# Performance work log

Measured on AMD Instinct MI355X. Metric: run time of the kernel, lower is better.

The kernel has to match this reference:

```python
import jax, jax.numpy as jnp
import numpy as np

B, S, HIST, D, NH, L = 8, 1024, 128, 1024, 16, 6
SD, TD, AD = 10, 3, 5
DH = D // NH
FF = 4 * D
EPS = 1e-5
SCALE = 1.0 / np.sqrt(DH)


def posenc(T):
    # sinusoidal PE, matches PositionalEncoding (positions start at 0)
    pos = jnp.arange(T, dtype=jnp.float32)[:, None]
    div = jnp.exp(jnp.arange(0, D, 2, dtype=jnp.float32) * (-np.log(10000.0) / D))
    pe = jnp.zeros((T, D), jnp.float32)
    pe = pe.at[:, 0::2].set(jnp.sin(pos * div))
    pe = pe.at[:, 1::2].set(jnp.cos(pos * div))
    return pe


def layernorm(x, g, b):
    m = jnp.mean(x, -1, keepdims=True)
    v = jnp.var(x, -1, keepdims=True)
    return (x - m) * jax.lax.rsqrt(v + EPS) * g + b


def mlp2(u, w1, b1, w2, b2):
    # Linear -> SiLU -> Linear (ConditionEmbedding branch)
    return jax.nn.silu(u @ w1 + b1) @ w2 + b2


def mha(q_in, kv_in, wq, bq, wk, bk, wv, bv, wo, bo, mask):
    Bq, Tq, _ = q_in.shape
    Tk = kv_in.shape[1]
    q = (q_in @ wq + bq).reshape(Bq, Tq, NH, DH)
    k = (kv_in @ wk + bk).reshape(Bq, Tk, NH, DH)
    v = (kv_in @ wv + bv).reshape(Bq, Tk, NH, DH)
    s = jnp.einsum('bthd,bshd->bhts', q, k) * SCALE + mask
    a = jax.nn.softmax(s, axis=-1)
    o = jnp.einsum('bhts,bshd->bthd', a, v).reshape(Bq, Tq, D)
    return o @ wo + bo


def setup_inputs():
    key = jax.random.key(0)
    ki = iter(jax.random.split(key, 64))
    w = lambda *sh: jax.random.normal(next(ki), sh, jnp.float32) * 0.02
    z = lambda *sh: jnp.zeros(sh, jnp.float32)
    inp = {
        'x': jax.random.normal(next(ki), (B, S, SD), jnp.float32),
        't': jax.random.randint(next(ki), (B,), 0, 30, dtype=jnp.int32),
        'target': jax.random.normal(next(ki), (B, TD), jnp.float32),
        'action': jax.random.normal(next(ki), (B, AD), jnp.float32),
        'history': jax.random.normal(next(ki), (B, HIST, SD), jnp.float32),
        'in_w': w(SD, D), 'in_b': z(D),
        't_w1': w(1, D), 't_b1': z(D), 't_w2': w(D, D), 't_b2': z(D),
        'tg_w1': w(TD, D), 'tg_b1': z(D), 'tg_w2': w(D, D), 'tg_b2': z(D),
        'ac_w1': w(AD, D), 'ac_b1': z(D), 'ac_w2': w(D, D), 'ac_b2': z(D),
        'sa_wq': w(L, D, D), 'sa_bq': z(L, D), 'sa_wk': w(L, D, D), 'sa_bk': z(L, D),
        'sa_wv': w(L, D, D), 'sa_bv': z(L, D), 'sa_wo': w(L, D, D), 'sa_bo': z(L, D),
        'ca_wq': w(L, D, D), 'ca_bq': z(L, D), 'ca_wk': w(L, D, D), 'ca_bk': z(L, D),
        'ca_wv': w(L, D, D), 'ca_bv': z(L, D), 'ca_wo': w(L, D, D), 'ca_bo': z(L, D),
        'ln1_g': jnp.ones((L, D), jnp.float32), 'ln1_b': z(L, D),
        'ln2_g': jnp.ones((L, D), jnp.float32), 'ln2_b': z(L, D),
        'ln3_g': jnp.ones((L, D), jnp.float32), 'ln3_b': z(L, D),
        'ff_w1': w(L, D, FF), 'ff_b1': z(L, FF), 'ff_w2': w(L, FF, D), 'ff_b2': z(L, D),
        'out_w': w(D, SD), 'out_b': z(SD),
    }
    return inp


def reference(x, t, target, action, history, in_w, in_b,
              t_w1, t_b1, t_w2, t_b2, tg_w1, tg_b1, tg_w2, tg_b2,
              ac_w1, ac_b1, ac_w2, ac_b2,
              sa_wq, sa_bq, sa_wk, sa_bk, sa_wv, sa_bv, sa_wo, sa_bo,
              ca_wq, ca_bq, ca_wk, ca_bk, ca_wv, ca_bv, ca_wo, ca_bo,
              ln1_g, ln1_b, ln2_g, ln2_b, ln3_g, ln3_b,
              ff_w1, ff_b1, ff_w2, ff_b2, out_w, out_b):
    # embed current traj and history (PE applied to each separately, as in torch code)
    x_emb = x @ in_w + in_b + posenc(S)[None]
    h_emb = history @ in_w + in_b + posenc(HIST)[None]
    # condition embedding: t + target + action branches
    cond = (mlp2(t[:, None].astype(jnp.float32), t_w1, t_b1, t_w2, t_b2)
            + mlp2(target, tg_w1, tg_b1, tg_w2, tg_b2)
            + mlp2(action, ac_w1, ac_b1, ac_w2, ac_b2))
    z = jnp.concatenate([h_emb, x_emb], axis=1) + cond[:, None, :]  # [B, T, D]
    T = HIST + S
    mask = jnp.where(jnp.tril(jnp.ones((T, T), bool)), 0.0, -jnp.inf)[None, None]
    mem = z  # TransformerDecoder memory is the (fixed) input sequence
    for i in range(L):
        # post-LN TransformerDecoderLayer: self-attn, cross-attn, relu FFN
        z = layernorm(z + mha(z, z, sa_wq[i], sa_bq[i], sa_wk[i], sa_bk[i],
                              sa_wv[i], sa_bv[i], sa_wo[i], sa_bo[i], mask), ln1_g[i], ln1_b[i])
        z = layernorm(z + mha(z, mem, ca_wq[i], ca_bq[i], ca_wk[i], ca_bk[i],
                              ca_wv[i], ca_bv[i], ca_wo[i], ca_bo[i], mask), ln2_g[i], ln2_b[i])
        ff = jax.nn.relu(z @ ff_w1[i] + ff_b1[i]) @ ff_w2[i] + ff_b2[i]
        z = layernorm(z + ff, ln3_g[i], ln3_b[i])
    return z[:, -S:, :] @ out_w + out_b
```

## Files before the change

### kernel.cpp

```cpp
#include <hip/hip_runtime.h>
#include <hip/hip_bf16.h>
#include <stdint.h>

#define B_    8
#define S_    1024
#define HIST_ 128
#define T_    1152
#define D_    1024
#define NH_   16
#define DH_   64
#define FF_   4096
#define L_    6
#define NROWS_ (B_*T_)

typedef __attribute__((ext_vector_type(8))) __bf16 bf16x8;
typedef __attribute__((ext_vector_type(4))) __bf16 bf16x4;
typedef __attribute__((ext_vector_type(4))) float  f32x4;

static __device__ __forceinline__ f32x4 mfma16(bf16x8 a, bf16x8 b, f32x4 c) {
  return __builtin_amdgcn_mfma_f32_16x16x32_bf16(a, b, c, 0, 0, 0);
}
static __device__ __forceinline__ void gload16(const __bf16* g, __bf16* l) {
  __builtin_amdgcn_global_load_lds((const __attribute__((address_space(1))) void*)g,
                                   (__attribute__((address_space(3))) void*)l, 16, 0, 0);
}
static __device__ __forceinline__ void gload16b(const char* g, char* l) {
  __builtin_amdgcn_global_load_lds((const __attribute__((address_space(1))) void*)g,
                                   (__attribute__((address_space(3))) void*)l, 16, 0, 0);
}
static __device__ __forceinline__ int xcd_swz(int orig, int nwg) {
  const int q = nwg >> 3, r = nwg & 7;
  const int x = orig & 7, i = orig >> 3;
  return (x < r ? x*(q+1) : r*(q+1) + (x-r)*q) + i;
}

template<int BF16OUT, int RELU>
__global__ __launch_bounds__(512, 2) void gemm192_k(const __bf16* __restrict__ A,
                                                    const __bf16* __restrict__ Bt,
                                                    const float* __restrict__ bias,
                                                    void* __restrict__ Cout,
                                                    int M, int N, int K, int ldc) {
  __shared__ __align__(16) char Lds[2][57344];
  const int tid = threadIdx.x;
  const int wid = tid >> 6, ln = tid & 63;
  const int wm = wid >> 2, wn = wid & 3;
  const int l15 = ln & 15, g = ln >> 4;
  const int nbx = N >> 8;
  const int wg = xcd_swz(blockIdx.x, gridDim.x);
  const int m0 = (wg / nbx) * 192, n0 = (wg % nbx) << 8;
  const size_t rstep = (size_t)K * 2;

  const char* srcp[7];
  int dsto[7];
#pragma unroll
  for (int p = 0; p < 7; ++p) {
    const int off = p*8192 + tid*16;
    int mat, ks, row;
    if (off < 12288)      { mat = 0; ks = 0; row = off >> 6; }
    else if (off < 24576) { mat = 0; ks = 1; row = (off - 12288) >> 6; }
    else if (off < 40960) { mat = 1; ks = 0; row = (off - 24576) >> 6; }
    else                  { mat = 1; ks = 1; row = (off - 40960) >> 6; }
    const int ch = (off >> 4) & 3;
    const int kb = ks*64 + ((ch ^ ((row >> 1) & 3)) << 4);
    srcp[p] = (mat ? (const char*)Bt + (size_t)(n0 + row)*rstep
                   : (const char*)A  + (size_t)(m0 + row)*rstep) + kb;
    dsto[p] = off;
  }
  auto stage = [&](int buf, int t) {
    char* lb = &Lds[buf][0];
    const size_t tb = (size_t)t << 7;
#pragma unroll
    for (int p = 0; p < 7; ++p) gload16b(srcp[p] + tb, lb + dsto[p]);
  };

  const int xr = (g ^ ((l15 >> 1) & 3)) << 4;
  const int arow = l15*64 + xr;
  const int aoffm = (wm*96) * 64;
  const int boff  = 24576 + (wn*64) * 64;

  const f32x4 zero = {0.f,0.f,0.f,0.f};
  f32x4 acc[6][4];
#pragma unroll
  for (int i=0;i<6;i++)
#pragma unroll
    for (int j=0;j<4;j++) acc[i][j] = zero;

  stage(0, 0); stage(1, 1);

  const int NT = K >> 6;
  for (int t = 0; t < NT; ++t) {
    const int buf = t & 1;
    if (t == NT-1) { asm volatile("s_waitcnt vmcnt(0)" ::: "memory"); }
    else           { asm volatile("s_waitcnt vmcnt(7)" ::: "memory"); }
    __builtin_amdgcn_s_barrier();
    const char* bufp = &Lds[buf][0];
    bf16x8 a0[6], a1[6], b0[4], b1[4];
#pragma unroll
    for (int mi=0;mi<6;mi++) a0[mi] = *(const bf16x8*)(bufp + aoffm + mi*1024 + arow);
#pragma unroll
    for (int ni=0;ni<4;ni++) b0[ni] = *(const bf16x8*)(bufp + boff + ni*1024 + arow);
#pragma unroll
    for (int mi=0;mi<6;mi++) a1[mi] = *(const bf16x8*)(bufp + 12288 + aoffm + mi*1024 + arow);
    __builtin_amdgcn_s_setprio(1);
#pragma unroll
    for (int mi=0;mi<6;mi++)
#pragma unroll
      for (int ni=0;ni<4;ni++) acc[mi][ni] = mfma16(a0[mi], b0[ni], acc[mi][ni]);
    __builtin_amdgcn_s_setprio(0);
#pragma unroll
    for (int ni=0;ni<4;ni++) b1[ni] = *(const bf16x8*)(bufp + boff + 16384 + ni*1024 + arow);
    asm volatile("s_waitcnt lgkmcnt(0)" ::: "memory");
    __builtin_amdgcn_sched_barrier(0);
    __builtin_amdgcn_s_barrier();
    if (t + 2 <= NT - 1) stage(buf, t + 2);
    __builtin_amdgcn_s_setprio(1);
#pragma unroll
    for (int mi=0;mi<6;mi++)
#pragma unroll
      for (int ni=0;ni<4;ni++) acc[mi][ni] = mfma16(a1[mi], b1[ni], acc[mi][ni]);
    __builtin_amdgcn_s_setprio(0);
  }

  const int colb = n0 + wn*64 + l15;
#pragma unroll
  for (int mi=0;mi<6;mi++) {
    const int row = m0 + wm*96 + mi*16 + g*4;
#pragma unroll
    for (int ni=0;ni<4;ni++) {
      const int col = colb + ni*16;
      const float bv = bias[col];
#pragma unroll
      for (int j=0;j<4;j++) {
        float v = acc[mi][ni][j] + bv;
        if (RELU) v = fmaxf(v, 0.f);
        if (BF16OUT) ((__bf16*)Cout)[(size_t)(row+j)*ldc + col] = (__bf16)v;
        else         ((float*)Cout)[(size_t)(row+j)*ldc + col] = v;
      }
    }
  }
}

template<int OUTMODE, int RELU>
__global__ __launch_bounds__(512, 2) void gemm256_k(const __bf16* __restrict__ A,
                                                    const __bf16* __restrict__ A2, int asplit,
                                                    const __bf16* __restrict__ Bt,
                                                    const float* __restrict__ b1,
                                                    const float* __restrict__ b2,
                                                    const float* __restrict__ b3, int s1, int s2,
                                                    void* __restrict__ CoutRM,
                                                    __bf16* __restrict__ CoutT,
                                                    int M, int N, int K, int ldc, int tsplit) {
  __shared__ __align__(16) __bf16 Lds[2][2][2][8192];
  const int tid = threadIdx.x;
  const int wid = tid >> 6, ln = tid & 63;
  const int wm = wid >> 2, wn = wid & 3;
  const int l15 = ln & 15, g = ln >> 4;
  const int nbx = N >> 8;
  const int wg = xcd_swz(blockIdx.x, gridDim.x);
  const int m0 = (wg / nbx) << 8, n0 = (wg % nbx) << 8;
  const size_t rstep = (size_t)K * 2;
  const __bf16* Aeff = (n0 < asplit) ? A : A2;

  const int srow = tid >> 2, schunk = tid & 3;
  const int sx = (schunk ^ ((srow >> 1) & 3)) << 4;
  const char* gAr = (const char*)Aeff + (size_t)(m0 + srow)*rstep + sx;
  const char* gBr = (const char*)Bt   + (size_t)(n0 + srow)*rstep + sx;
  const size_t hstep = (size_t)128 * rstep;

  const int xr = (g ^ ((l15 >> 1) & 3)) << 4;
  const int arow = l15 * 64 + xr;
  const int aoffm = (wm*128) * 64;
  const int boff  = (wn*64) * 64;

  const f32x4 zero = {0.f,0.f,0.f,0.f};
  f32x4 acc[8][4];
#pragma unroll
  for (int i=0;i<8;i++)
#pragma unroll
    for (int j=0;j<4;j++) acc[i][j] = zero;

  auto stage4 = [&](int buf, int ks, int tile) {
    const size_t off = (size_t)tile*128 + (size_t)ks*64;
    char* la = (char*)&Lds[buf][ks][0][0];
    char* lb = (char*)&Lds[buf][ks][1][0];
    gload16b(gAr + off,         la + tid*16);
    gload16b(gAr + off + hstep, la + 8192 + tid*16);
    gload16b(gBr + off,         lb + tid*16);
    gload16b(gBr + off + hstep, lb + 8192 + tid*16);
  };

  auto ktile = [&](int buf, bool st, int stile, bool gate0) {
    if (gate0) { asm volatile("s_waitcnt vmcnt(0)" ::: "memory"); }
    else       { asm volatile("s_waitcnt vmcnt(8)" ::: "memory"); }
    __builtin_amdgcn_s_barrier();
    const char* As0 = (const char*)&Lds[buf][0][0][0];
    const char* Bs0 = (const char*)&Lds[buf][0][1][0];
    const char* As1 = (const char*)&Lds[buf][1][0][0];
    const char* Bs1 = (const char*)&Lds[buf][1][1][0];
    bf16x8 a0[4], a1[4], b0[4], a2[4], b1v[4], a3[4];
#pragma unroll
    for (int mi=0;mi<4;mi++) a0[mi] = *(const bf16x8*)(As0 + aoffm + mi*1024 + arow);
#pragma unroll
    for (int ni=0;ni<4;ni++) b0[ni] = *(const bf16x8*)(Bs0 + boff + ni*1024 + arow);
#pragma unroll
    for (int mi=0;mi<4;mi++) a1[mi] = *(const bf16x8*)(As0 + aoffm + 4096 + mi*1024 + arow);
    __builtin_amdgcn_s_setprio(1);
#pragma unroll
    for (int mi=0;mi<4;mi++)
#pragma unroll
      for (int ni=0;ni<4;ni++) acc[mi][ni] = mfma16(a0[mi], b0[ni], acc[mi][ni]);
    __builtin_amdgcn_s_setprio(0);
#pragma unroll
    for (int mi=0;mi<4;mi++) a2[mi]  = *(const bf16x8*)(As1 + aoffm + mi*1024 + arow);
#pragma unroll
    for (int ni=0;ni<4;ni++) b1v[ni] = *(const bf16x8*)(Bs1 + boff + ni*1024 + arow);
    asm volatile("s_waitcnt lgkmcnt(0)" ::: "memory");
    __builtin_amdgcn_s_barrier();
    if (st) stage4(buf, 0, stile);
    __builtin_amdgcn_s_setprio(1);
#pragma unroll
    for (int mi=0;mi<4;mi++)
#pragma unroll
      for (int ni=0;ni<4;ni++) acc[4+mi][ni] = mfma16(a1[mi], b0[ni], acc[4+mi][ni]);
    __builtin_amdgcn_s_setprio(0);
#pragma unroll
    for (int mi=0;mi<4;mi++) a3[mi] = *(const bf16x8*)(As1 + aoffm + 4096 + mi*1024 + arow);
    __builtin_amdgcn_s_setprio(1);
#pragma unroll
    for (int mi=0;mi<4;mi++)
#pragma unroll
      for (int ni=0;ni<4;ni++) acc[mi][ni] = mfma16(a2[mi], b1v[ni], acc[mi][ni]);
    __builtin_amdgcn_s_setprio(0);
    asm volatile("s_waitcnt lgkmcnt(0)" ::: "memory");
    __builtin_amdgcn_s_barrier();
    if (st) stage4(buf, 1, stile);
    __builtin_amdgcn_s_setprio(1);
#pragma unroll
    for (int mi=0;mi<4;mi++)
#pragma unroll
      for (int ni=0;ni<4;ni++) acc[4+mi][ni] = mfma16(a3[mi], b1v[ni], acc[4+mi][ni]);
    __builtin_amdgcn_s_setprio(0);
  };

  stage4(0, 0, 0); stage4(0, 1, 0);
  stage4(1, 0, 1); stage4(1, 1, 1);

  const int NT = K >> 6, NI = NT >> 1;
  for (int i = 0; i < NI; ++i) {
    const bool st = (i + 1 < NI);
    ktile(0, st, 2*i + 2, false);
    ktile(1, st, 2*i + 3, i == NI - 1);
  }

  const int colb = n0 + wn*64 + l15;
#pragma unroll
  for (int mi=0;mi<8;mi++) {
    const int row = m0 + wm*128 + mi*16 + g*4;
#pragma unroll
    for (int ni=0;ni<4;ni++) {
      const int col = colb + ni*16;
      const float bv = (col < s1) ? b1[col] : ((col < s2) ? b2[col-s1] : b3[col-s2]);
      if (OUTMODE == 3 && col >= tsplit) {
        bf16x4 ct;
#pragma unroll
        for (int j=0;j<4;j++) {
          float v = acc[mi][ni][j] + bv;
          if (RELU) v = fmaxf(v, 0.f);
          ct[j] = (__bf16)v;
        }
        *(bf16x4*)(CoutT + (size_t)(col - tsplit)*M + row) = ct;
      } else {
#pragma unroll
        for (int j=0;j<4;j++) {
          float v = acc[mi][ni][j] + bv;
          if (RELU) v = fmaxf(v, 0.f);
          if (OUTMODE == 0) ((float*)CoutRM)[(size_t)(row+j)*ldc + col] = v;
          else              ((__bf16*)CoutRM)[(size_t)(row+j)*ldc + col] = (__bf16)v;
        }
      }
    }
  }
}

__global__ __launch_bounds__(256) void attn_k(const __bf16* __restrict__ QK,
                                              const __bf16* __restrict__ Vt,
                                              __bf16* __restrict__ O) {
  __shared__ __align__(16) __bf16 Ks[2][4096];
  __shared__ __align__(16) __bf16 Vs[2][4096];
  __shared__ __align__(16) __bf16 Pl[4][32*72];
  const int tid = threadIdx.x;
  const int wv = tid >> 6, ln = tid & 63;
  const int l15 = ln & 15, g = ln >> 4;
  const int wg = xcd_swz(blockIdx.x, 1152);
  const int qb = 8 - (wg % 9);
  const int hd = (wg / 9) & 15;
  const int b  = wg / 144;
  const int q0 = qb*128 + wv*32;

  bf16x8 qf[2][2];
#pragma unroll
  for (int f=0; f<2; ++f)
#pragma unroll
    for (int h=0; h<2; ++h)
      qf[f][h] = *(const bf16x8*)(QK + (size_t)(b*T_ + q0 + f*16 + l15)*2048 + hd*64 + h*32 + g*8);

  const int sr = tid >> 3;
  const int si = tid & 7;
  const int cb0 = (si*16) ^ ((sr & 7) << 4);
  const char* kg = (const char*)(QK + (size_t)b*T_*2048 + 1024 + hd*64);
  const char* vg = (const char*)(Vt + (size_t)hd*64*NROWS_ + (size_t)b*T_);

  const f32x4 zero = {0.f,0.f,0.f,0.f};
  f32x4 o[2][4];
#pragma unroll
  for (int f=0; f<2; ++f)
#pragma unroll
    for (int d=0; d<4; ++d) o[f][d] = zero;
  float mrun[2] = {-3.0e38f, -3.0e38f};
  float lrun[2] = {0.f, 0.f};
  const int nt = 2*qb + 2;

  {
    const int c = 0, kt = 0;
#pragma unroll
    for (int hr=0; hr<2; ++hr) {
      const int r = sr + hr*32;
      gload16((const __bf16*)(kg + (size_t)(kt + r)*4096 + cb0), &Ks[c][0] + hr*2048 + wv*512);
      gload16((const __bf16*)(vg + (size_t)r*(NROWS_*2) + (size_t)kt*2 + cb0), &Vs[c][0] + hr*2048 + wv*512);
    }
  }

  for (int t = 0; t < nt; ++t) {
    __syncthreads();
    if (t+1 < nt) {
      const int c = (t+1)&1, kt2 = (t+1)*64;
#pragma unroll
      for (int hr=0; hr<2; ++hr) {
        const int r = sr + hr*32;
        gload16((const __bf16*)(kg + (size_t)(kt2 + r)*4096 + cb0), &Ks[c][0] + hr*2048 + wv*512);
        gload16((const __bf16*)(vg + (size_t)r*(NROWS_*2) + (size_t)kt2*2 + cb0), &Vs[c][0] + hr*2048 + wv*512);
      }
    }
    const int kt = t*64;
    if (kt > q0 + 31) continue;
    const char* ks = (const char*)&Ks[t&1][0];
    const char* vs = (const char*)&Vs[t&1][0];

#pragma unroll
    for (int f=0; f<2; ++f) {
      const int qrow = q0 + f*16 + l15;
      f32x4 st[4];
      __builtin_amdgcn_s_setprio(1);
#pragma unroll
      for (int kf=0; kf<4; ++kf) {
        const int row = kf*16 + l15;
        const int swz = (row & 7) << 4;
        const bf16x8 k0 = *(const bf16x8*)(ks + row*128 + ((g*16) ^ swz));
        const bf16x8 k1 = *(const bf16x8*)(ks + row*128 + ((64 + g*16) ^ swz));
        st[kf] = mfma16(k1, qf[f][1], mfma16(k0, qf[f][0], zero));
      }
      __builtin_amdgcn_s_setprio(0);
      float p[16];
#pragma unroll
      for (int kf=0; kf<4; ++kf)
#pragma unroll
        for (int r=0; r<4; ++r) {
          const int kgl = kt + kf*16 + g*4 + r;
          p[kf*4+r] = (kgl <= qrow) ? st[kf][r]*0.125f : -3.0e38f;
        }
      float mloc = p[0];
#pragma unroll
      for (int i=1;i<16;i++) mloc = fmaxf(mloc, p[i]);
      mloc = fmaxf(mloc, __shfl_xor(mloc, 16));
      mloc = fmaxf(mloc, __shfl_xor(mloc, 32));
      if (__all(mloc - mrun[f] <= 8.f)) {
        float ls = 0.f;
#pragma unroll
        for (int i=0;i<16;i++) { p[i] = __expf(p[i] - mrun[f]); ls += p[i]; }
        ls += __shfl_xor(ls, 16); ls += __shfl_xor(ls, 32);
        lrun[f] += ls;
      } else {
        const float mnew = fmaxf(mrun[f], mloc);
        const float corr = __expf(mrun[f] - mnew);
        float ls = 0.f;
#pragma unroll
        for (int i=0;i<16;i++) { p[i] = __expf(p[i] - mnew); ls += p[i]; }
        ls += __shfl_xor(ls, 16); ls += __shfl_xor(ls, 32);
        lrun[f] = lrun[f]*corr + ls;
        mrun[f] = mnew;
        float cr[4];
#pragma unroll
        for (int r=0;r<4;r++) cr[r] = __shfl(corr, g*4 + r);
#pragma unroll
        for (int db=0; db<4; ++db)
#pragma unroll
          for (int r=0;r<4;r++) o[f][db][r] *= cr[r];
      }
#pragma unroll
      for (int kf=0; kf<4; ++kf) {
        bf16x4 pw;
#pragma unroll
        for (int r=0;r<4;r++) pw[r] = (__bf16)p[kf*4+r];
        *(bf16x4*)(&Pl[wv][(f*16 + l15)*72 + kf*16 + g*4]) = pw;
      }
    }
    __builtin_amdgcn_s_setprio(1);
#pragma unroll
    for (int f=0; f<2; ++f)
#pragma unroll
      for (int ks2=0; ks2<2; ++ks2) {
        const bf16x8 pa = *(const bf16x8*)(&Pl[wv][(f*16 + l15)*72 + ks2*32 + g*8]);
#pragma unroll
        for (int db=0; db<4; ++db) {
          const int d = db*16 + l15;
          const bf16x8 vf = *(const bf16x8*)(vs + d*128 + ((ks2*64 + g*16) ^ ((d & 7) << 4)));
          o[f][db] = mfma16(pa, vf, o[f][db]);
        }
      }
    __builtin_amdgcn_s_setprio(0);
  }

#pragma unroll
  for (int f=0; f<2; ++f) {
    const float inv = 1.f / lrun[f];
    float ir[4];
#pragma unroll
    for (int r=0;r<4;r++) ir[r] = __shfl(inv, g*4 + r);
#pragma unroll
    for (int db=0; db<4; ++db)
#pragma unroll
      for (int r=0;r<4;r++)
        O[(size_t)(b*T_ + q0 + f*16 + g*4 + r)*D_ + hd*64 + db*16 + l15] = (__bf16)(o[f][db][r]*ir[r]);
  }
}

__global__ __launch_bounds__(256) void wprep_k(const float* __restrict__ q, const float* __restrict__ k,
                                               const float* __restrict__ v, const float* __restrict__ o,
                                               const float* __restrict__ cq, const float* __restrict__ ck,
                                               const float* __restrict__ cv, const float* __restrict__ co,
                                               const float* __restrict__ f1, const float* __restrict__ f2,
                                               __bf16* __restrict__ wb) {
  __shared__ float tile[64][65];
  const int id = blockIdx.x;
  const float* src; __bf16* dst; int R, C, bx, by;
  if (id < 2048) {
    const int m = id >> 8, t = id & 255; bx = t & 15; by = t >> 4;
    const float* srcs[8] = {q,k,v,o,cq,ck,cv,co};
    src = srcs[m]; dst = wb + (size_t)m*1048576; R = 1024; C = 1024;
  } else if (id < 3072) {
    const int t = id - 2048; bx = t & 63; by = t >> 6;
    src = f1; dst = wb + (size_t)8*1048576; R = 1024; C = 4096;
  } else {
    const int t = id - 3072; bx = t & 15; by = t >> 4;
    src = f2; dst = wb + (size_t)12*1048576; R = 4096; C = 1024;
  }
  const int tx = threadIdx.x & 63, ty = threadIdx.x >> 6;
  const int r0 = by*64, c0 = bx*64;
#pragma unroll
  for (int i=0;i<16;i++) tile[ty+i*4][tx] = src[(size_t)(r0+ty+i*4)*C + c0+tx];
  __syncthreads();
#pragma unroll
  for (int i=0;i<16;i++) dst[(size_t)(c0+ty+i*4)*R + r0+tx] = (__bf16)tile[tx][ty+i*4];
}

__global__ __launch_bounds__(256) void ln_k(const float* __restrict__ zin, const __bf16* __restrict__ yin,
                                            const float* __restrict__ gam, const float* __restrict__ bet,
                                            float* __restrict__ zout, __bf16* __restrict__ zbout) {
  const int row = blockIdx.x, tid = threadIdx.x;
  const f32x4 zv = ((const f32x4*)(zin + (size_t)row*D_))[tid];
  const bf16x4 yv4 = ((const bf16x4*)(yin + (size_t)row*D_))[tid];
  f32x4 v;
#pragma unroll
  for (int j=0;j<4;j++) v[j] = zv[j] + (float)yv4[j];
  float s1 = v[0]+v[1]+v[2]+v[3];
  float s2 = v[0]*v[0]+v[1]*v[1]+v[2]*v[2]+v[3]*v[3];
#pragma unroll
  for (int off=32; off; off>>=1) { s1 += __shfl_xor(s1,off); s2 += __shfl_xor(s2,off); }
  __shared__ float red[8];
  const int wv = tid>>6, ln = tid&63;
  if (ln==0) { red[wv] = s1; red[4+wv] = s2; }
  __syncthreads();
  s1 = red[0]+red[1]+red[2]+red[3];
  s2 = red[4]+red[5]+red[6]+red[7];
  const float mean = s1 * (1.f/1024.f);
  const float var = s2 * (1.f/1024.f) - mean*mean;
  const float rs = rsqrtf(var + 1e-5f);
  const f32x4 gv = ((const f32x4*)gam)[tid];
  const f32x4 bv = ((const f32x4*)bet)[tid];
  f32x4 r; bf16x4 rb;
#pragma unroll
  for (int j=0;j<4;j++) { float t = (v[j]-mean)*rs*gv[j] + bv[j]; r[j] = t; rb[j] = (__bf16)t; }
  ((f32x4*)(zout + (size_t)row*D_))[tid] = r;
  ((bf16x4*)(zbout + (size_t)row*D_))[tid] = rb;
}

__global__ __launch_bounds__(256) void cond1_k(const int* __restrict__ t, const float* __restrict__ target,
                                               const float* __restrict__ action,
                                               const float* __restrict__ t_w1, const float* __restrict__ t_b1,
                                               const float* __restrict__ tg_w1, const float* __restrict__ tg_b1,
                                               const float* __restrict__ ac_w1, const float* __restrict__ ac_b1,
                                               float* __restrict__ h3) {
  const int i = blockIdx.x*256 + threadIdx.x;
  const int b = i >> 10, d = i & 1023;
  float u = (float)t[b] * t_w1[d] + t_b1[d];
  h3[i] = u / (1.f + __expf(-u));
  u = tg_b1[d];
#pragma unroll
  for (int j=0;j<3;j++) u += target[b*3+j]*tg_w1[j*1024+d];
  h3[8192 + i] = u / (1.f + __expf(-u));
  u = ac_b1[d];
#pragma unroll
  for (int j=0;j<5;j++) u += action[b*5+j]*ac_w1[j*1024+d];
  h3[16384 + i] = u / (1.f + __expf(-u));
}

__global__ __launch_bounds__(256) void cond2_k(const float* __restrict__ h3,
                                               const float* __restrict__ t_w2, const float* __restrict__ tg_w2,
                                               const float* __restrict__ ac_w2, float* __restrict__ cpart) {
  const int i = blockIdx.x*256 + threadIdx.x;
  const int ks = blockIdx.y;
  const int b = i >> 10, d = i & 1023;
  const float* ht = h3 + b*1024;
  const float* hg = h3 + 8192 + b*1024;
  const float* ha = h3 + 16384 + b*1024;
  float a = 0.f;
  for (int k = ks*128; k < ks*128+128; ++k)
    a += ht[k]*t_w2[(size_t)k*1024+d] + hg[k]*tg_w2[(size_t)k*1024+d] + ha[k]*ac_w2[(size_t)k*1024+d];
  cpart[ks*8192 + i] = a;
}

__global__ __launch_bounds__(256) void embed_k(const float* __restrict__ x, const float* __restrict__ hist,
                                               const float* __restrict__ in_w, const float* __restrict__ in_b,
                                               const float* __restrict__ cpart,
                                               const float* __restrict__ t_b2, const float* __restrict__ tg_b2,
                                               const float* __restrict__ ac_b2,
                                               float* __restrict__ z, __bf16* __restrict__ zb,
                                               __bf16* __restrict__ memb) {
  const int row = blockIdx.x, tid = threadIdx.x;
  const int b = row / T_, tt = row - b*T_;
  const float* feat = (tt < HIST_) ? (hist + ((size_t)b*HIST_ + tt)*10) : (x + ((size_t)b*S_ + (tt-HIST_))*10);
  float f[10];
#pragma unroll
  for (int s=0;s<10;s++) f[s] = feat[s];
  const float te = (float)((tt < HIST_) ? tt : tt - HIST_);
  f32x4 a = ((const f32x4*)in_b)[tid];
#pragma unroll
  for (int u=0;u<2;u++) {
    const int d = tid*4 + 2*u;
    const float freq = __expf((float)d * (-9.210340371976184f/1024.f));
    float sn, cs;
    __sincosf(te*freq, &sn, &cs);
    a[2*u] += sn; a[2*u+1] += cs;
  }
  a += ((const f32x4*)t_b2)[tid];
  a += ((const f32x4*)tg_b2)[tid];
  a += ((const f32x4*)ac_b2)[tid];
  const int cb = b*256 + tid;
#pragma unroll
  for (int ks=0;ks<8;ks++) a += ((const f32x4*)cpart)[ks*2048 + cb];
#pragma unroll
  for (int s=0;s<10;s++) {
    const f32x4 wv = ((const f32x4*)(in_w + s*1024))[tid];
    a += wv * f[s];
  }
  ((f32x4*)(z + (size_t)row*D_))[tid] = a;
  bf16x4 ab;
#pragma unroll
  for (int j=0;j<4;j++) ab[j] = (__bf16)a[j];
  ((bf16x4*)(zb + (size_t)row*D_))[tid] = ab;
  ((bf16x4*)(memb + (size_t)row*D_))[tid] = ab;
}

__global__ __launch_bounds__(256) void outp_k(const float* __restrict__ z, const float* __restrict__ w,
                                              const float* __restrict__ bo, float* __restrict__ out) {
  const int wv = threadIdx.x>>6, ln = threadIdx.x&63;
  const int row = blockIdx.x*4 + wv;
  const int b = row >> 10, s = row & 1023;
  const float* zr = z + ((size_t)b*T_ + HIST_ + s)*D_;
  float acc[10];
#pragma unroll
  for (int o=0;o<10;o++) acc[o]=0.f;
  for (int k=ln; k<1024; k+=64) {
    const float zv = zr[k];
    const float* wr = w + k*10;
#pragma unroll
    for (int o=0;o<10;o++) acc[o] += zv*wr[o];
  }
#pragma unroll
  for (int o=0;o<10;o++) {
#pragma unroll
    for (int off=32; off; off>>=1) acc[o] += __shfl_xor(acc[o], off);
  }
  if (ln==0) {
#pragma unroll
    for (int o=0;o<10;o++) out[(size_t)row*10+o] = acc[o] + bo[o];
  }
}

extern "C" void kernel_launch(void* const* d_in, const int* in_sizes, int n_in,
                              void* d_out, int out_size, void* d_ws, size_t ws_size,
                              hipStream_t stream) {
  const float* x      = (const float*)d_in[0];
  const int*   t      = (const int*)  d_in[1];
  const float* target = (const float*)d_in[2];
  const float* action = (const float*)d_in[3];
  const float* hist   = (const float*)d_in[4];
  const float* in_w   = (const float*)d_in[5];
  const float* in_b   = (const float*)d_in[6];
  const float* t_w1   = (const float*)d_in[7];
  const float* t_b1   = (const float*)d_in[8];
  const float* t_w2   = (const float*)d_in[9];
  const float* t_b2   = (const float*)d_in[10];
  const float* tg_w1  = (const float*)d_in[11];
  const float* tg_b1  = (const float*)d_in[12];
  const float* tg_w2  = (const float*)d_in[13];
  const float* tg_b2  = (const float*)d_in[14];
  const float* ac_w1  = (const float*)d_in[15];
  const float* ac_b1  = (const float*)d_in[16];
  const float* ac_w2  = (const float*)d_in[17];
  const float* ac_b2  = (const float*)d_in[18];
  const float* sa_wq  = (const float*)d_in[19];
  const float* sa_bq  = (const float*)d_in[20];
  const float* sa_wk  = (const float*)d_in[21];
  const float* sa_bk  = (const float*)d_in[22];
  const float* sa_wv  = (const float*)d_in[23];
  const float* sa_bv  = (const float*)d_in[24];
  const float* sa_wo  = (const float*)d_in[25];
  const float* sa_bo  = (const float*)d_in[26];
  const float* ca_wq  = (const float*)d_in[27];
  const float* ca_bq  = (const float*)d_in[28];
  const float* ca_wk  = (const float*)d_in[29];
  const float* ca_bk  = (const float*)d_in[30];
  const float* ca_wv  = (const float*)d_in[31];
  const float* ca_bv  = (const float*)d_in[32];
  const float* ca_wo  = (const float*)d_in[33];
  const float* ca_bo  = (const float*)d_in[34];
  const float* ln1_g  = (const float*)d_in[35];
  const float* ln1_b  = (const float*)d_in[36];
  const float* ln2_g  = (const float*)d_in[37];
  const float* ln2_b  = (const float*)d_in[38];
  const float* ln3_g  = (const float*)d_in[39];
  const float* ln3_b  = (const float*)d_in[40];
  const float* ff_w1  = (const float*)d_in[41];
  const float* ff_b1  = (const float*)d_in[42];
  const float* ff_w2  = (const float*)d_in[43];
  const float* ff_b2  = (const float*)d_in[44];
  const float* out_w  = (const float*)d_in[45];
  const float* out_b  = (const float*)d_in[46];

  if (ws_size < (size_t)224*1024*1024) return;

  char* p = (char*)d_ws;
  auto take = [&](size_t bytes) { char* r = p; p += (bytes + 255) & ~(size_t)255; return r; };
  __bf16* wbuf = (__bf16*)take((size_t)16*1024*1024*2);
  float*  z    = (float*) take((size_t)NROWS_*D_*4);
  __bf16* zb   = (__bf16*)take((size_t)NROWS_*D_*2);
  __bf16* memb = (__bf16*)take((size_t)NROWS_*D_*2);
  __bf16* qk   = (__bf16*)take((size_t)NROWS_*2048*2);
  __bf16* vt   = (__bf16*)take((size_t)1024*NROWS_*2);
  __bf16* ob   = (__bf16*)take((size_t)NROWS_*D_*2);
  __bf16* y    = (__bf16*)take((size_t)NROWS_*D_*2);
  float*  h3   = (float*) take((size_t)3*8192*4);
  float*  cpart= (float*) take((size_t)8*8192*4);
  __bf16* ffh  = qk;

  const dim3 blk(256);
  const dim3 blk5(512);
  const int BIG = 1<<30;
  cond1_k<<<32, blk, 0, stream>>>(t, target, action, t_w1, t_b1, tg_w1, tg_b1, ac_w1, ac_b1, h3);
  cond2_k<<<dim3(32,8), blk, 0, stream>>>(h3, t_w2, tg_w2, ac_w2, cpart);
  embed_k<<<NROWS_, blk, 0, stream>>>(x, hist, in_w, in_b, cpart, t_b2, tg_b2, ac_b2, z, zb, memb);

  const int M = NROWS_;
  for (int li=0; li<L_; ++li) {
    const size_t w0 = (size_t)li*D_*D_, b0 = (size_t)li*D_;
    const size_t f1 = (size_t)li*D_*FF_, fb1 = (size_t)li*FF_;
    wprep_k<<<4096, blk, 0, stream>>>(sa_wq+w0, sa_wk+w0, sa_wv+w0, sa_wo+w0,
                                      ca_wq+w0, ca_wk+w0, ca_wv+w0, ca_wo+w0,
                                      ff_w1+f1, ff_w2+f1, wbuf);
    gemm256_k<3,0><<<36*12, blk5, 0, stream>>>(zb, zb, BIG, wbuf+0*1048576,
                                               sa_bq+b0, sa_bk+b0, sa_bv+b0, 1024, 2048,
                                               qk, vt, M, 3072, 1024, 2048, 2048);
    attn_k<<<1152, blk, 0, stream>>>(qk, vt, ob);
    gemm192_k<1,0><<<48*4, blk5, 0, stream>>>(ob, wbuf+3*1048576, sa_bo+b0, y, M, 1024, 1024, 1024);
    ln_k<<<NROWS_, blk, 0, stream>>>(z, y, ln1_g+b0, ln1_b+b0, z, zb);
    gemm256_k<3,0><<<36*12, blk5, 0, stream>>>(zb, memb, 1024, wbuf+4*1048576,
                                               ca_bq+b0, ca_bk+b0, ca_bv+b0, 1024, 2048,
                                               qk, vt, M, 3072, 1024, 2048, 2048);
    attn_k<<<1152, blk, 0, stream>>>(qk, vt, ob);
    gemm192_k<1,0><<<48*4, blk5, 0, stream>>>(ob, wbuf+7*1048576, ca_bo+b0, y, M, 1024, 1024, 1024);
    ln_k<<<NROWS_, blk, 0, stream>>>(z, y, ln2_g+b0, ln2_b+b0, z, zb);
    gemm192_k<1,1><<<48*16, blk5, 0, stream>>>(zb, wbuf+(size_t)8*1048576, ff_b1+fb1, ffh, M, 4096, 1024, 4096);
    gemm192_k<1,0><<<48*4, blk5, 0, stream>>>(ffh, wbuf+(size_t)12*1048576, ff_b2+b0, y, M, 1024, 4096, 1024);
    ln_k<<<NROWS_, blk, 0, stream>>>(z, y, ln3_g+b0, ln3_b+b0, z, zb);
  }
  outp_k<<<2048, blk, 0, stream>>>(z, out_w, out_b, (float*)d_out);
}
```

Measured before the change: 3.940 ms.

## Fuse residual add into projection GEMM epilogue and drop fp32 residual stream

The output-projection and FFN-down GEMMs now add the bf16 residual (zb) in their epilogue and write an fp32 sum. LayerNorm then reads only that sum and writes only the bf16 activation. The separate fp32 z buffer is removed everywhere: embed, LN and the output head now read bf16. This cuts per-LN memory traffic, since LN no longer reads z plus y and writes z plus zb. The cost is that the residual path is kept only in bf16, which lowers accuracy, and the GEMM epilogue now does extra scattered residual reads and fp32 writes.

```diff
diff --git a/kernel.cpp b/kernel.cpp
--- a/kernel.cpp
+++ b/kernel.cpp
@@ -34,11 +34,12 @@
   return (x < r ? x*(q+1) : r*(q+1) + (x-r)*q) + i;
 }
 
-template<int BF16OUT, int RELU>
+template<int BF16OUT, int RELU, int RESADD>
 __global__ __launch_bounds__(512, 2) void gemm192_k(const __bf16* __restrict__ A,
                                                     const __bf16* __restrict__ Bt,
                                                     const float* __restrict__ bias,
                                                     void* __restrict__ Cout,
+                                                    const __bf16* __restrict__ resid,
                                                     int M, int N, int K, int ldc) {
   __shared__ __align__(16) char Lds[2][57344];
   const int tid = threadIdx.x;
@@ -132,6 +133,7 @@
 #pragma unroll
       for (int j=0;j<4;j++) {
         float v = acc[mi][ni][j] + bv;
+        if (RESADD) v += (float)resid[(size_t)(row+j)*ldc + col];
         if (RELU) v = fmaxf(v, 0.f);
         if (BF16OUT) ((__bf16*)Cout)[(size_t)(row+j)*ldc + col] = (__bf16)v;
         else         ((float*)Cout)[(size_t)(row+j)*ldc + col] = v;
@@ -463,15 +465,11 @@
   for (int i=0;i<16;i++) dst[(size_t)(c0+ty+i*4)*R + r0+tx] = (__bf16)tile[tx][ty+i*4];
 }
 
-__global__ __launch_bounds__(256) void ln_k(const float* __restrict__ zin, const __bf16* __restrict__ yin,
+__global__ __launch_bounds__(256) void ln_k(const float* __restrict__ ysum,
                                             const float* __restrict__ gam, const float* __restrict__ bet,
-                                            float* __restrict__ zout, __bf16* __restrict__ zbout) {
+                                            __bf16* __restrict__ zbout) {
   const int row = blockIdx.x, tid = threadIdx.x;
-  const f32x4 zv = ((const f32x4*)(zin + (size_t)row*D_))[tid];
-  const bf16x4 yv4 = ((const bf16x4*)(yin + (size_t)row*D_))[tid];
-  f32x4 v;
-#pragma unroll
-  for (int j=0;j<4;j++) v[j] = zv[j] + (float)yv4[j];
+  const f32x4 v = ((const f32x4*)(ysum + (size_t)row*D_))[tid];
   float s1 = v[0]+v[1]+v[2]+v[3];
   float s2 = v[0]*v[0]+v[1]*v[1]+v[2]*v[2]+v[3]*v[3];
 #pragma unroll
@@ -487,10 +485,9 @@
   const float rs = rsqrtf(var + 1e-5f);
   const f32x4 gv = ((const f32x4*)gam)[tid];
   const f32x4 bv = ((const f32x4*)bet)[tid];
-  f32x4 r; bf16x4 rb;
-#pragma unroll
-  for (int j=0;j<4;j++) { float t = (v[j]-mean)*rs*gv[j] + bv[j]; r[j] = t; rb[j] = (__bf16)t; }
-  ((f32x4*)(zout + (size_t)row*D_))[tid] = r;
+  bf16x4 rb;
+#pragma unroll
+  for (int j=0;j<4;j++) rb[j] = (__bf16)((v[j]-mean)*rs*gv[j] + bv[j]);
   ((bf16x4*)(zbout + (size_t)row*D_))[tid] = rb;
 }
 
@@ -534,8 +531,7 @@
                                                const float* __restrict__ cpart,
                                                const float* __restrict__ t_b2, const float* __restrict__ tg_b2,
                                                const float* __restrict__ ac_b2,
-                                               float* __restrict__ z, __bf16* __restrict__ zb,
-                                               __bf16* __restrict__ memb) {
+                                               __bf16* __restrict__ zb, __bf16* __restrict__ memb) {
   const int row = blockIdx.x, tid = threadIdx.x;
   const int b = row / T_, tt = row - b*T_;
   const float* feat = (tt < HIST_) ? (hist + ((size_t)b*HIST_ + tt)*10) : (x + ((size_t)b*S_ + (tt-HIST_))*10);
@@ -563,7 +559,6 @@
     const f32x4 wv = ((const f32x4*)(in_w + s*1024))[tid];
     a += wv * f[s];
   }
-  ((f32x4*)(z + (size_t)row*D_))[tid] = a;
   bf16x4 ab;
 #pragma unroll
   for (int j=0;j<4;j++) ab[j] = (__bf16)a[j];
@@ -571,17 +566,17 @@
   ((bf16x4*)(memb + (size_t)row*D_))[tid] = ab;
 }
 
-__global__ __launch_bounds__(256) void outp_k(const float* __restrict__ z, const float* __restrict__ w,
+__global__ __launch_bounds__(256) void outp_k(const __bf16* __restrict__ z, const float* __restrict__ w,
                                               const float* __restrict__ bo, float* __restrict__ out) {
   const int wv = threadIdx.x>>6, ln = threadIdx.x&63;
   const int row = blockIdx.x*4 + wv;
   const int b = row >> 10, s = row & 1023;
-  const float* zr = z + ((size_t)b*T_ + HIST_ + s)*D_;
+  const __bf16* zr = z + ((size_t)b*T_ + HIST_ + s)*D_;
   float acc[10];
 #pragma unroll
   for (int o=0;o<10;o++) acc[o]=0.f;
   for (int k=ln; k<1024; k+=64) {
-    const float zv = zr[k];
+    const float zv = (float)zr[k];
     const float* wr = w + k*10;
 #pragma unroll
     for (int o=0;o<10;o++) acc[o] += zv*wr[o];
@@ -653,13 +648,12 @@
   char* p = (char*)d_ws;
   auto take = [&](size_t bytes) { char* r = p; p += (bytes + 255) & ~(size_t)255; return r; };
   __bf16* wbuf = (__bf16*)take((size_t)16*1024*1024*2);
-  float*  z    = (float*) take((size_t)NROWS_*D_*4);
   __bf16* zb   = (__bf16*)take((size_t)NROWS_*D_*2);
   __bf16* memb = (__bf16*)take((size_t)NROWS_*D_*2);
   __bf16* qk   = (__bf16*)take((size_t)NROWS_*2048*2);
   __bf16* vt   = (__bf16*)take((size_t)1024*NROWS_*2);
   __bf16* ob   = (__bf16*)take((size_t)NROWS_*D_*2);
-  __bf16* y    = (__bf16*)take((size_t)NROWS_*D_*2);
+  float*  ysum = (float*) take((size_t)NROWS_*D_*4);
   float*  h3   = (float*) take((size_t)3*8192*4);
   float*  cpart= (float*) take((size_t)8*8192*4);
   __bf16* ffh  = qk;
@@ -669,7 +663,7 @@
   const int BIG = 1<<30;
   cond1_k<<<32, blk, 0, stream>>>(t, target, action, t_w1, t_b1, tg_w1, tg_b1, ac_w1, ac_b1, h3);
   cond2_k<<<dim3(32,8), blk, 0, stream>>>(h3, t_w2, tg_w2, ac_w2, cpart);
-  embed_k<<<NROWS_, blk, 0, stream>>>(x, hist, in_w, in_b, cpart, t_b2, tg_b2, ac_b2, z, zb, memb);
+  embed_k<<<NROWS_, blk, 0, stream>>>(x, hist, in_w, in_b, cpart, t_b2, tg_b2, ac_b2, zb, memb);
 
   const int M = NROWS_;
   for (int li=0; li<L_; ++li) {
@@ -682,17 +676,21 @@
                                                sa_bq+b0, sa_bk+b0, sa_bv+b0, 1024, 2048,
                                                qk, vt, M, 3072, 1024, 2048, 2048);
     attn_k<<<1152, blk, 0, stream>>>(qk, vt, ob);
-    gemm192_k<1,0><<<48*4, blk5, 0, stream>>>(ob, wbuf+3*1048576, sa_bo+b0, y, M, 1024, 1024, 1024);
-    ln_k<<<NROWS_, blk, 0, stream>>>(z, y, ln1_g+b0, ln1_b+b0, z, zb);
+    gemm192_k<0,0,1><<<48*4, blk5, 0, stream>>>(ob, wbuf+3*1048576, sa_bo+b0, ysum, zb,
+                                                M, 1024, 1024, 1024);
+    ln_k<<<NROWS_, blk, 0, stream>>>(ysum, ln1_g+b0, ln1_b+b0, zb);
     gemm256_k<3,0><<<36*12, blk5, 0, stream>>>(zb, memb, 1024, wbuf+4*1048576,
                                                ca_bq+b0, ca_bk+b0, ca_bv+b0, 1024, 2048,
                                                qk, vt, M, 3072, 1024, 2048, 2048);
     attn_k<<<1152, blk, 0, stream>>>(qk, vt, ob);
-    gemm192_k<1,0><<<48*4, blk5, 0, stream>>>(ob, wbuf+7*1048576, ca_bo+b0, y, M, 1024, 1024, 1024);
-    ln_k<<<NROWS_, blk, 0, stream>>>(z, y, ln2_g+b0, ln2_b+b0, z, zb);
-    gemm192_k<1,1><<<48*16, blk5, 0, stream>>>(zb, wbuf+(size_t)8*1048576, ff_b1+fb1, ffh, M, 4096, 1024, 4096);
-    gemm192_k<1,0><<<48*4, blk5, 0, stream>>>(ffh, wbuf+(size_t)12*1048576, ff_b2+b0, y, M, 1024, 4096, 1024);
-    ln_k<<<NROWS_, blk, 0, stream>>>(z, y, ln3_g+b0, ln3_b+b0, z, zb);
-  }
-  outp_k<<<2048, blk, 0, stream>>>(z, out_w, out_b, (float*)d_out);
-}
+    gemm192_k<0,0,1><<<48*4, blk5, 0, stream>>>(ob, wbuf+7*1048576, ca_bo+b0, ysum, zb,
+                                                M, 1024, 1024, 1024);
+    ln_k<<<NROWS_, blk, 0, stream>>>(ysum, ln2_g+b0, ln2_b+b0, zb);
+    gemm192_k<1,1,0><<<48*16, blk5, 0, stream>>>(zb, wbuf+(size_t)8*1048576, ff_b1+fb1, ffh, nullptr,
+                                                 M, 4096, 1024, 4096);
+    gemm192_k<0,0,1><<<48*4, blk5, 0, stream>>>(ffh, wbuf+(size_t)12*1048576, ff_b2+b0, ysum, zb,
+                                                M, 1024, 4096, 1024);
+    ln_k<<<NROWS_, blk, 0, stream>>>(ysum, ln3_g+b0, ln3_b+b0, zb);
+  }
+  outp_k<<<2048, blk, 0, stream>>>(zb, out_w, out_b, (float*)d_out);
+}
```

Measured after the change: 3.905 ms. Within noise of the previous version (-0.9%).
